# Optimization experiments

Measured on AMD Instinct MI355X. Metric: run time of the kernel, lower is better.

Reference implementation:

```python
import jax, jax.numpy as jnp
import numpy as np

P_FACTOR = 3.0
EPS = 1e-12  # torch F.normalize eps


def _l2norm(x):
    # F.normalize(x, dim=1): divide by max(||x||_2, eps) along feature dim
    n = jnp.sqrt(jnp.sum(x * x, axis=1, keepdims=True))
    return x / jnp.maximum(n, EPS)


def setup_inputs() -> dict:
    key = jax.random.key(0)
    ks = jax.random.split(key, 7)
    B, N, F, E = 4096, 20000, 768, 512
    X = jax.random.normal(ks[0], (B, F), jnp.float32)
    D = jax.random.normal(ks[1], (N, F), jnp.float32)
    r = jax.random.uniform(ks[2], (N, 1), jnp.float32)  # correctness in [0,1]
    g_w = jax.random.normal(ks[3], (E, F), jnp.float32) * (1.0 / np.sqrt(F))
    g_b = jax.random.normal(ks[4], (E,), jnp.float32) * 0.01
    h_w = jax.random.normal(ks[5], (1, 1), jnp.float32)
    h_b = jax.random.normal(ks[6], (1,), jnp.float32) * 0.01
    return {"X": X, "D": D, "r": r, "g_w": g_w, "g_b": g_b, "h_w": h_w, "h_b": h_b}


def reference(X, D, r, g_w, g_b, h_w, h_b):
    # register_buffer path: r = ex_correct * 2 - 1
    r = r * 2.0 - 1.0
    # g: Linear(feat_dim -> feat_embed_dim) on both queries and exemplars
    Xe = X @ g_w.T + g_b            # [B, E]
    De = D @ g_w.T + g_b            # [N, E]
    # h: Linear(1 -> class_embed_dim)
    rh = r @ h_w.T + h_b            # [N, C]
    # Minerva: cosine similarity -> power-law activation -> weighted retrieval
    a = _l2norm(Xe) @ _l2norm(De).T                 # [B, N]
    a = jnp.sign(a) * jnp.abs(a) ** P_FACTOR        # |s|^p * sign(s)
    logits = a @ rh                                 # [B, C]
    preds = jax.nn.sigmoid(logits)
    return logits, preds
```

## Files before the change

### kernel.cpp

```cpp
#include <hip/hip_runtime.h>
#include <cstdint>


typedef __attribute__((ext_vector_type(4))) float  f32x4;
typedef __attribute__((ext_vector_type(8))) __bf16 bf16x8;
typedef __attribute__((ext_vector_type(4))) __bf16 bf16x4;

constexpr int B = 4096, N = 20000, F = 768, E = 512;

#define AS1CAST(p) ((__attribute__((address_space(1))) unsigned int*)(uintptr_t)(p))
#define AS3CAST(p) ((__attribute__((address_space(3))) unsigned int*)(uintptr_t)(p))

__device__ __forceinline__ void gload_lds16(const void* g, void* l) {
  __builtin_amdgcn_global_load_lds(AS1CAST(g), AS3CAST(l), 16, 0, 0);
}


__global__ void k_prep(const float* __restrict__ G, const float* __restrict__ r,
                       const float* __restrict__ hw, const float* __restrict__ hb,
                       __bf16* __restrict__ Gb, float* __restrict__ rh,
                       float* __restrict__ lg, float* __restrict__ norm2) {
  const int t = blockIdx.x * blockDim.x + threadIdx.x;
  constexpr int nG = E * F / 4;
  if (t < nG) {
    float4 v = ((const float4*)G)[t];
    bf16x4 o;
    o[0] = (__bf16)v.x; o[1] = (__bf16)v.y; o[2] = (__bf16)v.z; o[3] = (__bf16)v.w;
    ((bf16x4*)Gb)[t] = o;
  }
  if (t < N) rh[t] = (2.0f * r[t] - 1.0f) * hw[0] + hb[0];
  if (t < B) lg[t] = 0.0f;
  if (t < B + N) norm2[t] = 0.0f;
}


__global__ __launch_bounds__(256, 3)
void k_embed(const float* __restrict__ Xf, const float* __restrict__ Df,
             const __bf16* __restrict__ Gb, const float* __restrict__ bias,
             __bf16* __restrict__ Eb, float* __restrict__ norm2) {
  constexpr int K = F;
  __shared__ __bf16 As[128 * 64];
  __shared__ __bf16 Bs[128 * 64];
  __shared__ float ssum[128];
  const int tid  = threadIdx.x;
  const int wave = tid >> 6;
  const int lane = tid & 63;
  const int by = blockIdx.y;
  const bool isX = (by < B / 128);
  const float* A = isX ? Xf : Df;
  const int m0 = isX ? by * 128 : (by - B / 128) * 128;
  const int Mr = isX ? B : N;
  const int g0 = by * 128;
  const int n0 = blockIdx.x * 128;
  if (tid < 128) ssum[tid] = 0.0f;

  const int srow = tid >> 3;
  const int scg  = (tid & 7) ^ (srow & 7);
  const float*  ga[4];
  const __bf16* gb[4];
  __bf16* la[4];
  __bf16* lb[4];
#pragma unroll
  for (int q = 0; q < 4; ++q) {
    const int row = srow + q * 32;
    int arow = m0 + row; if (arow >= Mr) arow = Mr - 1;
    const int brow = n0 + row;
    ga[q] = A  + (size_t)arow * K + scg * 8;
    gb[q] = Gb + (size_t)brow * K + scg * 8;
    la[q] = &As[q * 2048 + tid * 8];
    lb[q] = &Bs[q * 2048 + tid * 8];
  }

  const int mw = (wave & 1) * 64;
  const int nw = (wave >> 1) * 64;
  const int quad = lane >> 4;
  const int l15  = lane & 15;
  f32x4 acc[4][4] = {};

  float4 av[4][2];
#pragma unroll
  for (int q = 0; q < 4; ++q) {
    av[q][0] = *(const float4*)(ga[q]);
    av[q][1] = *(const float4*)(ga[q] + 4);
  }

#pragma unroll 1
  for (int kb = 0; kb < K; kb += 64) {
#pragma unroll
    for (int q = 0; q < 4; ++q) gload_lds16(gb[q] + kb, lb[q]);
#pragma unroll
    for (int q = 0; q < 4; ++q) {
      bf16x8 o;
      o[0] = (__bf16)av[q][0].x; o[1] = (__bf16)av[q][0].y;
      o[2] = (__bf16)av[q][0].z; o[3] = (__bf16)av[q][0].w;
      o[4] = (__bf16)av[q][1].x; o[5] = (__bf16)av[q][1].y;
      o[6] = (__bf16)av[q][1].z; o[7] = (__bf16)av[q][1].w;
      *(bf16x8*)la[q] = o;
    }
    if (kb + 64 < K) {
#pragma unroll
      for (int q = 0; q < 4; ++q) {
        av[q][0] = *(const float4*)(ga[q] + kb + 64);
        av[q][1] = *(const float4*)(ga[q] + kb + 68);
      }
    }
    __syncthreads();
#pragma unroll
    for (int h = 0; h < 2; ++h) {
      bf16x8 af[4], bfr[4];
#pragma unroll
      for (int i = 0; i < 4; ++i) {
        const int rr = mw + i * 16 + l15;
        af[i] = *(const bf16x8*)&As[rr * 64 + ((quad + h * 4) ^ (rr & 7)) * 8];
      }
#pragma unroll
      for (int j = 0; j < 4; ++j) {
        const int rr = nw + j * 16 + l15;
        bfr[j] = *(const bf16x8*)&Bs[rr * 64 + ((quad + h * 4) ^ (rr & 7)) * 8];
      }
#pragma unroll
      for (int i = 0; i < 4; ++i)
#pragma unroll
        for (int j = 0; j < 4; ++j)
          acc[i][j] = __builtin_amdgcn_mfma_f32_16x16x32_bf16(af[i], bfr[j], acc[i][j], 0, 0, 0);
    }
    __syncthreads();
  }

#pragma unroll
  for (int i = 0; i < 4; ++i) {
    float part[4] = {0.0f, 0.0f, 0.0f, 0.0f};
#pragma unroll
    for (int j = 0; j < 4; ++j) {
      const int col = n0 + nw + j * 16 + l15;
      const float bv = bias[col];
#pragma unroll
      for (int rr = 0; rr < 4; ++rr) {
        const int row = mw + i * 16 + quad * 4 + rr;
        if (m0 + row < Mr) {
          const __bf16 hv = (__bf16)(acc[i][j][rr] + bv);
          Eb[(size_t)(g0 + row) * E + col] = hv;
          const float vb = (float)hv;
          part[rr] += vb * vb;
        }
      }
    }
#pragma unroll
    for (int rr = 0; rr < 4; ++rr) {
      float v = part[rr];
      v += __shfl_xor(v, 1);
      v += __shfl_xor(v, 2);
      v += __shfl_xor(v, 4);
      v += __shfl_xor(v, 8);
      if (l15 == 0) atomicAdd(&ssum[mw + i * 16 + quad * 4 + rr], v);
    }
  }
  __syncthreads();
  if (tid < 128 && m0 + tid < Mr) atomicAdd(&norm2[g0 + tid], ssum[tid]);
}


__global__ void k_weights(const float* __restrict__ norm2, const float* __restrict__ rh,
                          float* __restrict__ ix3, float* __restrict__ wcol) {
  const int t = blockIdx.x * blockDim.x + threadIdx.x;
  if (t < B) {
    const float ix = 1.0f / fmaxf(sqrtf(norm2[t]), 1e-12f);
    ix3[t] = ix * ix * ix;
  }
  if (t < N) {
    const float id = 1.0f / fmaxf(sqrtf(norm2[B + t]), 1e-12f);
    wcol[t] = id * id * id * rh[t];
  }
}


__global__ __launch_bounds__(256, 4)
void k_minerva(const __bf16* __restrict__ Xe, const __bf16* __restrict__ De,
               const float* __restrict__ ix3a, const float* __restrict__ wcol,
               float* __restrict__ logits) {
  constexpr int K  = 512;
  constexpr int MT = B / 128;
  constexpr int NT = (N + 127) / 128;
  constexpr int W  = 20;
  __shared__ __bf16 As[128 * 64];
  __shared__ __bf16 Bs[128 * 64];
  __shared__ float lsum[128];
  const int tid  = threadIdx.x;
  const int lane = tid & 63;
  const int wave = tid >> 6;

  const int bid   = blockIdx.x;
  const int panel = bid / (W * MT);
  const int bn    = panel * W;
  const int rem   = bid - panel * (W * MT);
  const int mt    = rem % MT;
  const int nt    = bn + rem / MT;
  const int m0 = mt * 128, n0 = nt * 128;
  if (tid < 128) lsum[tid] = 0.0f;

  const int srow = tid >> 3;
  const int scg  = (tid & 7) ^ (srow & 7);
  const __bf16* ga[4];
  const __bf16* gb[4];
  __bf16* la[4];
  __bf16* lb[4];
#pragma unroll
  for (int q = 0; q < 4; ++q) {
    const int row = srow + q * 32;
    const int arow = m0 + row;
    int brow = n0 + row; if (brow >= N) brow = N - 1;
    ga[q] = Xe + (size_t)arow * K + scg * 8;
    gb[q] = De + (size_t)brow * K + scg * 8;
    la[q] = &As[q * 2048 + tid * 8];
    lb[q] = &Bs[q * 2048 + tid * 8];
  }

  const int mw = (wave & 1) * 64;
  const int nw = (wave >> 1) * 64;
  const int quad = lane >> 4;
  const int l15  = lane & 15;
  f32x4 acc[4][4] = {};

  for (int kb = 0; kb < K; kb += 64) {
#pragma unroll
    for (int q = 0; q < 4; ++q) gload_lds16(ga[q] + kb, la[q]);
#pragma unroll
    for (int q = 0; q < 4; ++q) gload_lds16(gb[q] + kb, lb[q]);
    __syncthreads();
#pragma unroll
    for (int h = 0; h < 2; ++h) {
      bf16x8 af[4], bfr[4];
#pragma unroll
      for (int i = 0; i < 4; ++i) {
        const int rr = mw + i * 16 + l15;
        af[i] = *(const bf16x8*)&As[rr * 64 + ((quad + h * 4) ^ (rr & 7)) * 8];
      }
#pragma unroll
      for (int j = 0; j < 4; ++j) {
        const int rr = nw + j * 16 + l15;
        bfr[j] = *(const bf16x8*)&Bs[rr * 64 + ((quad + h * 4) ^ (rr & 7)) * 8];
      }
#pragma unroll
      for (int i = 0; i < 4; ++i)
#pragma unroll
        for (int j = 0; j < 4; ++j)
          acc[i][j] = __builtin_amdgcn_mfma_f32_16x16x32_bf16(af[i], bfr[j], acc[i][j], 0, 0, 0);
    }
    __syncthreads();
  }

  float w4[4];
#pragma unroll
  for (int j = 0; j < 4; ++j) {
    const int col = n0 + nw + j * 16 + l15;
    w4[j] = (col < N) ? wcol[col] : 0.0f;
  }
#pragma unroll
  for (int i = 0; i < 4; ++i) {
    float x3[4];
#pragma unroll
    for (int rr = 0; rr < 4; ++rr)
      x3[rr] = ix3a[m0 + mw + i * 16 + quad * 4 + rr];
    float part[4] = {0.0f, 0.0f, 0.0f, 0.0f};
#pragma unroll
    for (int j = 0; j < 4; ++j)
#pragma unroll
      for (int rr = 0; rr < 4; ++rr) {
        const float a = acc[i][j][rr];
        const float a2 = a * a;
        part[rr] = fmaf(a2 * a, w4[j], part[rr]);
      }
#pragma unroll
    for (int rr = 0; rr < 4; ++rr) {
      float v = part[rr] * x3[rr];
      v += __shfl_xor(v, 1);
      v += __shfl_xor(v, 2);
      v += __shfl_xor(v, 4);
      v += __shfl_xor(v, 8);
      if (l15 == 0) atomicAdd(&lsum[mw + i * 16 + quad * 4 + rr], v);
    }
  }
  __syncthreads();
  if (tid < 128) atomicAdd(&logits[m0 + tid], lsum[tid]);
}


__global__ void k_finalize(const float* __restrict__ logits, float* __restrict__ out, int n) {
  int i = blockIdx.x * blockDim.x + threadIdx.x;
  if (i < n) {
    float L = logits[i];
    out[i] = L;
    out[n + i] = 1.0f / (1.0f + expf(-L));
  }
}


extern "C" void kernel_launch(void* const* d_in, const int* in_sizes, int n_in,
                              void* d_out, int out_size, void* d_ws, size_t ws_size,
                              hipStream_t stream) {
  const float* X   = (const float*)d_in[0];
  const float* D   = (const float*)d_in[1];
  const float* r   = (const float*)d_in[2];
  const float* g_w = (const float*)d_in[3];
  const float* g_b = (const float*)d_in[4];
  const float* h_w = (const float*)d_in[5];
  const float* h_b = (const float*)d_in[6];
  float* out = (float*)d_out;

  char* ws = (char*)d_ws;
  __bf16* Gb    = (__bf16*)(ws + 0);
  __bf16* Eb    = (__bf16*)(ws + 786432);
  float*  rh    = (float*) (ws + 25460736);
  float*  norm2 = (float*) (ws + 25540736);
  float*  lg    = (float*) (ws + 25637120);
  float*  ix3   = (float*) (ws + 25653504);
  float*  wcol  = (float*) (ws + 25669888);

  k_prep<<<384, 256, 0, stream>>>(g_w, r, h_w, h_b, Gb, rh, lg, norm2);

  k_embed<<<dim3(E / 128, B / 128 + (N + 127) / 128), 256, 0, stream>>>(
      X, D, Gb, g_b, Eb, norm2);

  k_weights<<<(N + 255) / 256, 256, 0, stream>>>(norm2, rh, ix3, wcol);

  k_minerva<<<157 * 32, 256, 0, stream>>>(Eb, Eb + (size_t)B * E, ix3, wcol, lg);

  k_finalize<<<(B + 255) / 256, 256, 0, stream>>>(lg, out, B);
}
```

Measured before the change: 255.5 us.

## Double-buffer LDS tiles in embedding GEMM to overlap loads with MFMA

The embedding GEMM kernel now keeps two LDS buffers for the A and B tiles. The next K-tile's B data (async global-to-LDS) and A data (global fp32 loads) are issued before the MFMAs on the current tile, and the bf16-converted A is written into the other buffer afterwards. This leaves one barrier per iteration instead of two and hides global load latency behind compute. In exchange LDS use doubles and the launch-bounds occupancy hint drops from 3 to 2 blocks per CU.

```diff
diff --git a/kernel.cpp b/kernel.cpp
--- a/kernel.cpp
+++ b/kernel.cpp
@@ -34,13 +34,14 @@
 }
 
 
-__global__ __launch_bounds__(256, 3)
+__global__ __launch_bounds__(256, 2)
 void k_embed(const float* __restrict__ Xf, const float* __restrict__ Df,
              const __bf16* __restrict__ Gb, const float* __restrict__ bias,
              __bf16* __restrict__ Eb, float* __restrict__ norm2) {
-  constexpr int K = F;
-  __shared__ __bf16 As[128 * 64];
-  __shared__ __bf16 Bs[128 * 64];
+  constexpr int K  = F;
+  constexpr int NK = K / 64;
+  __shared__ __bf16 As[2][128 * 64];
+  __shared__ __bf16 Bs[2][128 * 64];
   __shared__ float ssum[128];
   const int tid  = threadIdx.x;
   const int wave = tid >> 6;
@@ -58,8 +59,7 @@
   const int scg  = (tid & 7) ^ (srow & 7);
   const float*  ga[4];
   const __bf16* gb[4];
-  __bf16* la[4];
-  __bf16* lb[4];
+  int lo[4];
 #pragma unroll
   for (int q = 0; q < 4; ++q) {
     const int row = srow + q * 32;
@@ -67,8 +67,7 @@
     const int brow = n0 + row;
     ga[q] = A  + (size_t)arow * K + scg * 8;
     gb[q] = Gb + (size_t)brow * K + scg * 8;
-    la[q] = &As[q * 2048 + tid * 8];
-    lb[q] = &Bs[q * 2048 + tid * 8];
+    lo[q] = q * 2048 + tid * 8;
   }
 
   const int mw = (wave & 1) * 64;
@@ -77,52 +76,70 @@
   const int l15  = lane & 15;
   f32x4 acc[4][4] = {};
 
-  float4 av[4][2];
-#pragma unroll
-  for (int q = 0; q < 4; ++q) {
-    av[q][0] = *(const float4*)(ga[q]);
-    av[q][1] = *(const float4*)(ga[q] + 4);
-  }
-
-#pragma unroll 1
-  for (int kb = 0; kb < K; kb += 64) {
-#pragma unroll
-    for (int q = 0; q < 4; ++q) gload_lds16(gb[q] + kb, lb[q]);
+#pragma unroll
+  for (int q = 0; q < 4; ++q) gload_lds16(gb[q], &Bs[0][lo[q]]);
+  {
+    float4 a0[4][2];
+#pragma unroll
+    for (int q = 0; q < 4; ++q) {
+      a0[q][0] = *(const float4*)(ga[q]);
+      a0[q][1] = *(const float4*)(ga[q] + 4);
+    }
 #pragma unroll
     for (int q = 0; q < 4; ++q) {
       bf16x8 o;
-      o[0] = (__bf16)av[q][0].x; o[1] = (__bf16)av[q][0].y;
-      o[2] = (__bf16)av[q][0].z; o[3] = (__bf16)av[q][0].w;
-      o[4] = (__bf16)av[q][1].x; o[5] = (__bf16)av[q][1].y;
-      o[6] = (__bf16)av[q][1].z; o[7] = (__bf16)av[q][1].w;
-      *(bf16x8*)la[q] = o;
-    }
-    if (kb + 64 < K) {
+      o[0] = (__bf16)a0[q][0].x; o[1] = (__bf16)a0[q][0].y;
+      o[2] = (__bf16)a0[q][0].z; o[3] = (__bf16)a0[q][0].w;
+      o[4] = (__bf16)a0[q][1].x; o[5] = (__bf16)a0[q][1].y;
+      o[6] = (__bf16)a0[q][1].z; o[7] = (__bf16)a0[q][1].w;
+      *(bf16x8*)&As[0][lo[q]] = o;
+    }
+  }
+  __syncthreads();
+
+#pragma unroll 1
+  for (int t = 0; t < NK; ++t) {
+    const int cur = t & 1, nxt = cur ^ 1;
+    const int kb2 = (t + 1) * 64;
+    float4 av[4][2];
+    if (t + 1 < NK) {
+#pragma unroll
+      for (int q = 0; q < 4; ++q) gload_lds16(gb[q] + kb2, &Bs[nxt][lo[q]]);
 #pragma unroll
       for (int q = 0; q < 4; ++q) {
-        av[q][0] = *(const float4*)(ga[q] + kb + 64);
-        av[q][1] = *(const float4*)(ga[q] + kb + 68);
-      }
-    }
-    __syncthreads();
+        av[q][0] = *(const float4*)(ga[q] + kb2);
+        av[q][1] = *(const float4*)(ga[q] + kb2 + 4);
+      }
+    }
 #pragma unroll
     for (int h = 0; h < 2; ++h) {
       bf16x8 af[4], bfr[4];
 #pragma unroll
       for (int i = 0; i < 4; ++i) {
         const int rr = mw + i * 16 + l15;
-        af[i] = *(const bf16x8*)&As[rr * 64 + ((quad + h * 4) ^ (rr & 7)) * 8];
+        af[i] = *(const bf16x8*)&As[cur][rr * 64 + ((quad + h * 4) ^ (rr & 7)) * 8];
       }
 #pragma unroll
       for (int j = 0; j < 4; ++j) {
         const int rr = nw + j * 16 + l15;
-        bfr[j] = *(const bf16x8*)&Bs[rr * 64 + ((quad + h * 4) ^ (rr & 7)) * 8];
+        bfr[j] = *(const bf16x8*)&Bs[cur][rr * 64 + ((quad + h * 4) ^ (rr & 7)) * 8];
       }
 #pragma unroll
       for (int i = 0; i < 4; ++i)
 #pragma unroll
         for (int j = 0; j < 4; ++j)
           acc[i][j] = __builtin_amdgcn_mfma_f32_16x16x32_bf16(af[i], bfr[j], acc[i][j], 0, 0, 0);
+    }
+    if (t + 1 < NK) {
+#pragma unroll
+      for (int q = 0; q < 4; ++q) {
+        bf16x8 o;
+        o[0] = (__bf16)av[q][0].x; o[1] = (__bf16)av[q][0].y;
+        o[2] = (__bf16)av[q][0].z; o[3] = (__bf16)av[q][0].w;
+        o[4] = (__bf16)av[q][1].x; o[5] = (__bf16)av[q][1].y;
+        o[6] = (__bf16)av[q][1].z; o[7] = (__bf16)av[q][1].w;
+        *(bf16x8*)&As[nxt][lo[q]] = o;
+      }
     }
     __syncthreads();
   }
```

New measurement: 268.0 us. 1.05x slower.
